# Kernel optimization log

Measured on AMD Instinct MI355X. Metric: run time of the kernel, lower is better.

The kernel has to match this reference:

```python
import jax, jax.numpy as jnp
import numpy as np

NUM_HEADS = 12
SCALE = 0.125  # (C // num_heads) ** -0.5 = 64 ** -0.5


def setup_inputs() -> dict:
    key = jax.random.key(0)
    k1, k2, k3, k4, k5 = jax.random.split(key, 5)
    B, N, C = 8, 1024, 768
    x = jax.random.normal(k1, (B, N, C), dtype=jnp.float32)
    qkv_w = jax.random.normal(k2, (3 * C, C), dtype=jnp.float32) * (C ** -0.5)
    qkv_b = jax.random.normal(k3, (3 * C,), dtype=jnp.float32) * 0.02
    proj_w = jax.random.normal(k4, (C, C), dtype=jnp.float32) * (C ** -0.5)
    proj_b = jax.random.normal(k5, (C,), dtype=jnp.float32) * 0.02
    return {"x": x, "qkv_w": qkv_w, "qkv_b": qkv_b,
            "proj_w": proj_w, "proj_b": proj_b, "H": 32, "W": 32}


def reference(x, qkv_w, qkv_b, proj_w, proj_b, H, W):
    B, N, C = x.shape
    hd = C // NUM_HEADS
    # qkv: [B, N, 3C] -> [3, B, heads, N, hd]
    qkv = (x @ qkv_w.T + qkv_b).reshape(B, N, 3, NUM_HEADS, hd)
    qkv = jnp.transpose(qkv, (2, 0, 3, 1, 4))
    q, k, v = qkv[0], qkv[1], qkv[2]
    # attention scores [B, heads, N, N]
    attn = jnp.einsum('bhnd,bhmd->bhnm', q, k) * SCALE
    attn = jax.nn.softmax(attn, axis=-1)
    # attn_drop / proj_drop are identity in eval mode
    out = jnp.einsum('bhnm,bhmd->bhnd', attn, v)
    out = jnp.transpose(out, (0, 2, 1, 3)).reshape(B, N, C)
    out = out @ proj_w.T + proj_b
    return out
```

## Files before the change

kernel.cpp:

```cpp
#include <hip/hip_runtime.h>
#include <math.h>

#define NSEQ  1024
#define CDIM  768
#define NH    12
#define HD    64
#define QS    6291456
#define EXPC  0.18033688011112042f

typedef __bf16 bf16x8 __attribute__((ext_vector_type(8)));
typedef float  f32x4  __attribute__((ext_vector_type(4)));

__device__ __forceinline__ unsigned short f2bf(float f) {
    union { float f; unsigned u; } v; v.f = f;
    unsigned r = v.u + 0x7FFFu + ((v.u >> 16) & 1u);
    return (unsigned short)(r >> 16);
}

#if __has_builtin(__builtin_amdgcn_cvt_pk_bf16_f32)
typedef __bf16 bf16x2 __attribute__((ext_vector_type(2)));
__device__ __forceinline__ void store_p4(unsigned short* pr, int row16,
                                         float p0, float p1, float p2, float p3) {
    union { bf16x2 v; unsigned u; } a, b;
    a.v = __builtin_amdgcn_cvt_pk_bf16_f32(p0, p1);
    b.v = __builtin_amdgcn_cvt_pk_bf16_f32(p2, p3);
    pr[row16]      = (unsigned short)(a.u);
    pr[16 + row16] = (unsigned short)(a.u >> 16);
    pr[32 + row16] = (unsigned short)(b.u);
    pr[48 + row16] = (unsigned short)(b.u >> 16);
}
#else
__device__ __forceinline__ void store_p4(unsigned short* pr, int row16,
                                         float p0, float p1, float p2, float p3) {
    pr[row16]      = f2bf(p0);
    pr[16 + row16] = f2bf(p1);
    pr[32 + row16] = f2bf(p2);
    pr[48 + row16] = f2bf(p3);
}
#endif

__device__ __forceinline__ void gld_lds16(const unsigned short* g, unsigned short* l) {
    __builtin_amdgcn_global_load_lds(
        (const __attribute__((address_space(1))) void*)g,
        (__attribute__((address_space(3))) void*)l, 16, 0, 0);
}

__global__ __launch_bounds__(256) void cvt_all(const float* __restrict__ x,
                                               const float* __restrict__ w1,
                                               const float* __restrict__ w2,
                                               unsigned short* __restrict__ xb,
                                               unsigned short* __restrict__ w1b,
                                               unsigned short* __restrict__ w2b,
                                               int n0, int n1, int n2) {
    int i = (blockIdx.x * 256 + threadIdx.x) * 4;
    const float* s; unsigned short* d; int off;
    if (i < n0)           { s = x;  d = xb;  off = i; }
    else if (i < n0 + n1) { s = w1; d = w1b; off = i - n0; }
    else if (i < n0 + n1 + n2) { s = w2; d = w2b; off = i - n0 - n1; }
    else return;
    float4 v = *(const float4*)(s + off);
    ushort4 o;
    o.x = f2bf(v.x); o.y = f2bf(v.y); o.z = f2bf(v.z); o.w = f2bf(v.w);
    *(ushort4*)(d + off) = o;
}

template <int MODE>
__global__ __launch_bounds__(256) void mfma_gemm_bt(const unsigned short* __restrict__ A,
                                                    const unsigned short* __restrict__ Bw,
                                                    const float* __restrict__ bias,
                                                    void* __restrict__ outp,
                                                    int M, int N, int K) {
    __shared__ unsigned short smem[4 * 128 * 32];

    const int tid = threadIdx.x;
    const int wave = tid >> 6, lane = tid & 63;
    const int row16 = lane & 15, quad = lane >> 4;
    const int wm = (wave >> 1) * 64, wn = (wave & 1) * 64;
    const int m0 = blockIdx.x * 128, n0 = blockIdx.y * 128;

    const int srow0 = (tid * 8) >> 5,         scol0 = (tid * 8) & 31;
    const int srow1 = ((tid + 256) * 8) >> 5, scol1 = ((tid + 256) * 8) & 31;

    f32x4 acc[4][4];
#pragma unroll
    for (int i = 0; i < 4; ++i)
#pragma unroll
        for (int j = 0; j < 4; ++j) acc[i][j] = (f32x4){0.f, 0.f, 0.f, 0.f};

    gld_lds16(&A[(size_t)(m0 + srow0) * K + scol0], &smem[wave * 512]);
    gld_lds16(&A[(size_t)(m0 + srow1) * K + scol1], &smem[2048 + wave * 512]);
    gld_lds16(&Bw[(size_t)(n0 + srow0) * K + scol0], &smem[8192 + wave * 512]);
    gld_lds16(&Bw[(size_t)(n0 + srow1) * K + scol1], &smem[8192 + 2048 + wave * 512]);

    const int nk = K / 32;
    for (int ki = 0; ki < nk; ++ki) {
        const int co = (ki & 1) * 4096;
        const int no = 4096 - co;
        __syncthreads();
        if (ki + 1 < nk) {
            const int k0 = (ki + 1) * 32;
            gld_lds16(&A[(size_t)(m0 + srow0) * K + k0 + scol0], &smem[no + wave * 512]);
            gld_lds16(&A[(size_t)(m0 + srow1) * K + k0 + scol1], &smem[no + 2048 + wave * 512]);
            gld_lds16(&Bw[(size_t)(n0 + srow0) * K + k0 + scol0], &smem[8192 + no + wave * 512]);
            gld_lds16(&Bw[(size_t)(n0 + srow1) * K + k0 + scol1], &smem[8192 + no + 2048 + wave * 512]);
        }
        bf16x8 af[4], bfr[4];
#pragma unroll
        for (int mt = 0; mt < 4; ++mt)
            af[mt] = *(const bf16x8*)&smem[co + (wm + mt * 16 + row16) * 32 + quad * 8];
#pragma unroll
        for (int nt = 0; nt < 4; ++nt)
            bfr[nt] = *(const bf16x8*)&smem[8192 + co + (wn + nt * 16 + row16) * 32 + quad * 8];
#pragma unroll
        for (int mt = 0; mt < 4; ++mt)
#pragma unroll
            for (int nt = 0; nt < 4; ++nt)
                acc[mt][nt] = __builtin_amdgcn_mfma_f32_16x16x32_bf16(af[mt], bfr[nt], acc[mt][nt], 0, 0, 0);
    }

    float bias4[4];
#pragma unroll
    for (int nt = 0; nt < 4; ++nt) bias4[nt] = bias[n0 + wn + nt * 16 + row16];

    if (MODE == 0) {
#pragma unroll
        for (int mt = 0; mt < 4; ++mt)
#pragma unroll
            for (int nt = 0; nt < 4; ++nt)
#pragma unroll
                for (int r = 0; r < 4; ++r) {
                    int grow = m0 + wm + mt * 16 + quad * 4 + r;
                    int gcol = n0 + wn + nt * 16 + row16;
                    ((float*)outp)[(size_t)grow * N + gcol] = acc[mt][nt][r] + bias4[nt];
                }
    } else {
        unsigned short* qkvb = (unsigned short*)outp;
        __syncthreads();
#pragma unroll
        for (int mt = 0; mt < 4; ++mt)
#pragma unroll
            for (int nt = 0; nt < 4; ++nt)
#pragma unroll
                for (int r = 0; r < 4; ++r)
                    smem[(wm + mt * 16 + quad * 4 + r) * 128 + wn + nt * 16 + row16] =
                        f2bf(acc[mt][nt][r] + bias4[nt]);
        __syncthreads();
#pragma unroll
        for (int i = 0; i < 8; ++i) {
            int u4 = i * 256 + tid;
            int row = u4 >> 4;
            int c8 = u4 & 15;
            int grow = m0 + row;
            int gcol = n0 + c8 * 8;
            int t = gcol / CDIM;
            int rr = gcol - t * CDIM;
            int h = rr >> 6, d = rr & 63;
            int b = grow >> 10, n = grow & 1023;
            *(uint4*)&qkvb[(size_t)t * QS + ((((size_t)b * NH + h) << 10) + n) * 64 + d] =
                *(const uint4*)&smem[row * 128 + c8 * 8];
        }
    }
}

__global__ __launch_bounds__(256, 4) void attn_mfma(const unsigned short* __restrict__ qkv,
                                                    unsigned short* __restrict__ abuf) {
    __shared__ unsigned short Ks[64 * 72];
    __shared__ unsigned short Vt[64 * 72];
    __shared__ unsigned short Ps[4][32 * 72];

    const int tid = threadIdx.x;
    const int wave = tid >> 6, lane = tid & 63;
    const int row16 = lane & 15, quad = lane >> 4;
    const int bid = blockIdx.x;
    const int xcd = bid & 7;
    const int local = bid >> 3;
    const int bh = xcd * 12 + (local >> 3);
    const int qt = local & 7;

    const unsigned short* Qg = qkv + (size_t)bh * NSEQ * HD + (size_t)qt * 128 * HD;
    const unsigned short* Kg = qkv + (size_t)QS + (size_t)bh * NSEQ * HD;
    const unsigned short* Vg = qkv + (size_t)2 * QS + (size_t)bh * NSEQ * HD;

    bf16x8 aq[2][2];
#pragma unroll
    for (int mt = 0; mt < 2; ++mt)
#pragma unroll
        for (int kst = 0; kst < 2; ++kst)
            aq[mt][kst] = *(const bf16x8*)&Qg[(size_t)(wave * 32 + mt * 16 + row16) * 64 +
                                              kst * 32 + quad * 8];

    f32x4 o[2][4];
    float l_i[2][4];
#pragma unroll
    for (int mt = 0; mt < 2; ++mt)
#pragma unroll
        for (int j = 0; j < 4; ++j) {
            o[mt][j] = (f32x4){0.f, 0.f, 0.f, 0.f};
            l_i[mt][j] = 0.f;
        }

    const int krow0 = (tid * 8) >> 6,  kcol0 = (tid * 8) & 63;
    const int krow1 = ((tid + 256) * 8) >> 6, kcol1 = ((tid + 256) * 8) & 63;
    const int kpair = tid & 31;
    const int colc = tid >> 5;

    uint4 ka = *(const uint4*)&Kg[(size_t)krow0 * 64 + kcol0];
    uint4 kb = *(const uint4*)&Kg[(size_t)krow1 * 64 + kcol1];
    uint4 va = *(const uint4*)&Vg[(size_t)(2 * kpair) * 64 + colc * 8];
    uint4 vb = *(const uint4*)&Vg[(size_t)(2 * kpair + 1) * 64 + colc * 8];

    for (int kt = 0; kt < 16; ++kt) {
        __syncthreads();
        *(uint4*)&Ks[krow0 * 72 + kcol0] = ka;
        *(uint4*)&Ks[krow1 * 72 + kcol1] = kb;
        {
            const unsigned short* a16 = (const unsigned short*)&va;
            const unsigned short* b16 = (const unsigned short*)&vb;
            unsigned int* vt32 = (unsigned int*)Vt;
#pragma unroll
            for (int j = 0; j < 8; ++j)
                vt32[(colc * 8 + j) * 36 + kpair] =
                    (unsigned int)a16[j] | ((unsigned int)b16[j] << 16);
        }
        __syncthreads();

        if (kt < 15) {
            const unsigned short* kn = Kg + (size_t)(kt + 1) * 64 * 64;
            const unsigned short* vn = Vg + (size_t)(kt + 1) * 64 * 64;
            ka = *(const uint4*)&kn[(size_t)krow0 * 64 + kcol0];
            kb = *(const uint4*)&kn[(size_t)krow1 * 64 + kcol1];
            va = *(const uint4*)&vn[(size_t)(2 * kpair) * 64 + colc * 8];
            vb = *(const uint4*)&vn[(size_t)(2 * kpair + 1) * 64 + colc * 8];
        }

        f32x4 s[2][4];
#pragma unroll
        for (int mt = 0; mt < 2; ++mt)
#pragma unroll
            for (int nt = 0; nt < 4; ++nt) s[mt][nt] = (f32x4){0.f, 0.f, 0.f, 0.f};
#pragma unroll
        for (int kst = 0; kst < 2; ++kst) {
            bf16x8 bk[4];
#pragma unroll
            for (int nt = 0; nt < 4; ++nt)
                bk[nt] = *(const bf16x8*)&Ks[(nt * 16 + row16) * 72 + kst * 32 + quad * 8];
#pragma unroll
            for (int mt = 0; mt < 2; ++mt)
#pragma unroll
                for (int nt = 0; nt < 4; ++nt)
                    s[mt][nt] = __builtin_amdgcn_mfma_f32_16x16x32_bf16(aq[mt][kst], bk[nt], s[mt][nt], 0, 0, 0);
        }

#pragma unroll
        for (int mt = 0; mt < 2; ++mt)
#pragma unroll
            for (int r = 0; r < 4; ++r) {
                float p0 = __builtin_amdgcn_exp2f(s[mt][0][r] * EXPC);
                float p1 = __builtin_amdgcn_exp2f(s[mt][1][r] * EXPC);
                float p2 = __builtin_amdgcn_exp2f(s[mt][2][r] * EXPC);
                float p3 = __builtin_amdgcn_exp2f(s[mt][3][r] * EXPC);
                l_i[mt][r] += (p0 + p1) + (p2 + p3);
                store_p4(&Ps[wave][(mt * 16 + quad * 4 + r) * 72], row16, p0, p1, p2, p3);
            }

#pragma unroll
        for (int kst = 0; kst < 2; ++kst) {
            bf16x8 ap[2], bv[4];
#pragma unroll
            for (int mt = 0; mt < 2; ++mt)
                ap[mt] = *(const bf16x8*)&Ps[wave][(mt * 16 + row16) * 72 + kst * 32 + quad * 8];
#pragma unroll
            for (int dt = 0; dt < 4; ++dt)
                bv[dt] = *(const bf16x8*)&Vt[(dt * 16 + row16) * 72 + kst * 32 + quad * 8];
#pragma unroll
            for (int mt = 0; mt < 2; ++mt)
#pragma unroll
                for (int dt = 0; dt < 4; ++dt)
                    o[mt][dt] = __builtin_amdgcn_mfma_f32_16x16x32_bf16(ap[mt], bv[dt], o[mt][dt], 0, 0, 0);
        }
    }

    const int b = bh / NH, h = bh - b * NH;
#pragma unroll
    for (int mt = 0; mt < 2; ++mt)
#pragma unroll
        for (int r = 0; r < 4; ++r) {
            float l = l_i[mt][r];
            l += __shfl_xor(l, 1);
            l += __shfl_xor(l, 2);
            l += __shfl_xor(l, 4);
            l += __shfl_xor(l, 8);
            float inv = 1.f / l;
            int n = qt * 128 + wave * 32 + mt * 16 + quad * 4 + r;
            size_t base = ((size_t)(b * NSEQ + n)) * CDIM + h * HD;
#pragma unroll
            for (int dt = 0; dt < 4; ++dt)
                abuf[base + dt * 16 + row16] = f2bf(o[mt][dt][r] * inv);
        }
}

extern "C" void kernel_launch(void* const* d_in, const int* in_sizes, int n_in,
                              void* d_out, int out_size, void* d_ws, size_t ws_size,
                              hipStream_t stream) {
    const float* x      = (const float*)d_in[0];
    const float* qkv_w  = (const float*)d_in[1];
    const float* qkv_b  = (const float*)d_in[2];
    const float* proj_w = (const float*)d_in[3];
    const float* proj_b = (const float*)d_in[4];
    float* out = (float*)d_out;

    const int M = 8 * NSEQ;
    unsigned short* ws = (unsigned short*)d_ws;
    unsigned short* xb   = ws;
    unsigned short* wq   = xb + (size_t)M * CDIM;
    unsigned short* wp   = wq + (size_t)3 * CDIM * CDIM;
    unsigned short* qkvb = wp + (size_t)CDIM * CDIM;
    unsigned short* ab   = qkvb + (size_t)3 * QS;

    const int nx = M * CDIM, nq = 3 * CDIM * CDIM, np = CDIM * CDIM;
    cvt_all<<<(nx + nq + np) / 1024, 256, 0, stream>>>(x, qkv_w, proj_w, xb, wq, wp,
                                                       nx, nq, np);

    mfma_gemm_bt<1><<<dim3(M / 128, (3 * CDIM) / 128), 256, 0, stream>>>(
        xb, wq, qkv_b, qkvb, M, 3 * CDIM, CDIM);

    attn_mfma<<<dim3(8 * NH * (NSEQ / 128)), 256, 0, stream>>>(qkvb, ab);

    mfma_gemm_bt<0><<<dim3(M / 128, CDIM / 128), 256, 0, stream>>>(
        ab, wp, proj_b, out, M, CDIM, CDIM);
}
```

Before: 195.6 us.

## Use 256x128 tiles for QKV GEMM and transpose attention score MFMA for packed P stores

Splits the GEMM template into a projection kernel and a dedicated QKV kernel. The QKV kernel uses 256x128 block tiles with each wave computing 64x128, which gives more B-tile reuse but uses more accumulator registers. The epilogue writes to LDS in two passes. In attention, S is computed as K·Q^T so each lane holds four consecutive key columns, allowing packed 8-byte stores of P to LDS instead of scattered 2-byte stores. The row-sum reduction changes to match the new layout.

```diff
diff --git a/kernel.cpp b/kernel.cpp
--- a/kernel.cpp
+++ b/kernel.cpp
@@ -19,23 +19,16 @@
 
 #if __has_builtin(__builtin_amdgcn_cvt_pk_bf16_f32)
 typedef __bf16 bf16x2 __attribute__((ext_vector_type(2)));
-__device__ __forceinline__ void store_p4(unsigned short* pr, int row16,
-                                         float p0, float p1, float p2, float p3) {
+__device__ __forceinline__ uint2 pack4bf(float p0, float p1, float p2, float p3) {
     union { bf16x2 v; unsigned u; } a, b;
     a.v = __builtin_amdgcn_cvt_pk_bf16_f32(p0, p1);
     b.v = __builtin_amdgcn_cvt_pk_bf16_f32(p2, p3);
-    pr[row16]      = (unsigned short)(a.u);
-    pr[16 + row16] = (unsigned short)(a.u >> 16);
-    pr[32 + row16] = (unsigned short)(b.u);
-    pr[48 + row16] = (unsigned short)(b.u >> 16);
+    return make_uint2(a.u, b.u);
 }
 #else
-__device__ __forceinline__ void store_p4(unsigned short* pr, int row16,
-                                         float p0, float p1, float p2, float p3) {
-    pr[row16]      = f2bf(p0);
-    pr[16 + row16] = f2bf(p1);
-    pr[32 + row16] = f2bf(p2);
-    pr[48 + row16] = f2bf(p3);
+__device__ __forceinline__ uint2 pack4bf(float p0, float p1, float p2, float p3) {
+    return make_uint2((unsigned)f2bf(p0) | ((unsigned)f2bf(p1) << 16),
+                      (unsigned)f2bf(p2) | ((unsigned)f2bf(p3) << 16));
 }
 #endif
 
@@ -64,12 +57,11 @@
     *(ushort4*)(d + off) = o;
 }
 
-template <int MODE>
-__global__ __launch_bounds__(256) void mfma_gemm_bt(const unsigned short* __restrict__ A,
-                                                    const unsigned short* __restrict__ Bw,
-                                                    const float* __restrict__ bias,
-                                                    void* __restrict__ outp,
-                                                    int M, int N, int K) {
+__global__ __launch_bounds__(256) void gemm_proj(const unsigned short* __restrict__ A,
+                                                 const unsigned short* __restrict__ Bw,
+                                                 const float* __restrict__ bias,
+                                                 float* __restrict__ out,
+                                                 int M, int N, int K) {
     __shared__ unsigned short smem[4 * 128 * 32];
 
     const int tid = threadIdx.x;
@@ -122,35 +114,107 @@
 #pragma unroll
     for (int nt = 0; nt < 4; ++nt) bias4[nt] = bias[n0 + wn + nt * 16 + row16];
 
-    if (MODE == 0) {
+#pragma unroll
+    for (int mt = 0; mt < 4; ++mt)
+#pragma unroll
+        for (int nt = 0; nt < 4; ++nt)
+#pragma unroll
+            for (int r = 0; r < 4; ++r) {
+                int grow = m0 + wm + mt * 16 + quad * 4 + r;
+                int gcol = n0 + wn + nt * 16 + row16;
+                out[(size_t)grow * N + gcol] = acc[mt][nt][r] + bias4[nt];
+            }
+}
+
+__global__ __launch_bounds__(256) void gemm_qkv(const unsigned short* __restrict__ A,
+                                                const unsigned short* __restrict__ Bw,
+                                                const float* __restrict__ bias,
+                                                unsigned short* __restrict__ qkvb,
+                                                int M, int N, int K) {
+    __shared__ unsigned short smem[2 * 12288];
+
+    const int tid = threadIdx.x;
+    const int wave = tid >> 6, lane = tid & 63;
+    const int row16 = lane & 15, quad = lane >> 4;
+    const int m0 = blockIdx.x * 256, n0 = blockIdx.y * 128;
+
+    f32x4 acc[4][8];
+#pragma unroll
+    for (int i = 0; i < 4; ++i)
+#pragma unroll
+        for (int j = 0; j < 8; ++j) acc[i][j] = (f32x4){0.f, 0.f, 0.f, 0.f};
+
+#pragma unroll
+    for (int i = 0; i < 4; ++i) {
+        const int flat = (tid + i * 256) * 8;
+        gld_lds16(&A[(size_t)(m0 + (flat >> 5)) * K + (flat & 31)],
+                  &smem[i * 2048 + wave * 512]);
+    }
+#pragma unroll
+    for (int i = 0; i < 2; ++i) {
+        const int flat = (tid + i * 256) * 8;
+        gld_lds16(&Bw[(size_t)(n0 + (flat >> 5)) * K + (flat & 31)],
+                  &smem[8192 + i * 2048 + wave * 512]);
+    }
+
+    const int nk = K / 32;
+    for (int ki = 0; ki < nk; ++ki) {
+        const int co = (ki & 1) * 12288;
+        const int no = 12288 - co;
+        __syncthreads();
+        if (ki + 1 < nk) {
+            const int k0 = (ki + 1) * 32;
+#pragma unroll
+            for (int i = 0; i < 4; ++i) {
+                const int flat = (tid + i * 256) * 8;
+                gld_lds16(&A[(size_t)(m0 + (flat >> 5)) * K + k0 + (flat & 31)],
+                          &smem[no + i * 2048 + wave * 512]);
+            }
+#pragma unroll
+            for (int i = 0; i < 2; ++i) {
+                const int flat = (tid + i * 256) * 8;
+                gld_lds16(&Bw[(size_t)(n0 + (flat >> 5)) * K + k0 + (flat & 31)],
+                          &smem[no + 8192 + i * 2048 + wave * 512]);
+            }
+        }
+        bf16x8 af[4], bfr[8];
 #pragma unroll
         for (int mt = 0; mt < 4; ++mt)
-#pragma unroll
-            for (int nt = 0; nt < 4; ++nt)
-#pragma unroll
-                for (int r = 0; r < 4; ++r) {
-                    int grow = m0 + wm + mt * 16 + quad * 4 + r;
-                    int gcol = n0 + wn + nt * 16 + row16;
-                    ((float*)outp)[(size_t)grow * N + gcol] = acc[mt][nt][r] + bias4[nt];
-                }
-    } else {
-        unsigned short* qkvb = (unsigned short*)outp;
-        __syncthreads();
+            af[mt] = *(const bf16x8*)&smem[co + (wave * 64 + mt * 16 + row16) * 32 + quad * 8];
+#pragma unroll
+        for (int nt = 0; nt < 8; ++nt)
+            bfr[nt] = *(const bf16x8*)&smem[co + 8192 + (nt * 16 + row16) * 32 + quad * 8];
 #pragma unroll
         for (int mt = 0; mt < 4; ++mt)
 #pragma unroll
-            for (int nt = 0; nt < 4; ++nt)
-#pragma unroll
-                for (int r = 0; r < 4; ++r)
-                    smem[(wm + mt * 16 + quad * 4 + r) * 128 + wn + nt * 16 + row16] =
-                        f2bf(acc[mt][nt][r] + bias4[nt]);
+            for (int nt = 0; nt < 8; ++nt)
+                acc[mt][nt] = __builtin_amdgcn_mfma_f32_16x16x32_bf16(af[mt], bfr[nt], acc[mt][nt], 0, 0, 0);
+    }
+
+    float bias8[8];
+#pragma unroll
+    for (int nt = 0; nt < 8; ++nt) bias8[nt] = bias[n0 + nt * 16 + row16];
+
+#pragma unroll
+    for (int p = 0; p < 2; ++p) {
+        __syncthreads();
+        if ((wave >> 1) == p) {
+#pragma unroll
+            for (int mt = 0; mt < 4; ++mt)
+#pragma unroll
+                for (int nt = 0; nt < 8; ++nt)
+#pragma unroll
+                    for (int r = 0; r < 4; ++r)
+                        smem[((wave & 1) * 64 + mt * 16 + quad * 4 + r) * 128 + nt * 16 + row16] =
+                            f2bf(acc[mt][nt][r] + bias8[nt]);
+        }
         __syncthreads();
 #pragma unroll
         for (int i = 0; i < 8; ++i) {
             int u4 = i * 256 + tid;
             int row = u4 >> 4;
             int c8 = u4 & 15;
-            int grow = m0 + row;
+            int grow = m0 + p * 128 + row;
             int gcol = n0 + c8 * 8;
             int t = gcol / CDIM;
             int rr = gcol - t * CDIM;
@@ -190,14 +254,11 @@
                                               kst * 32 + quad * 8];
 
     f32x4 o[2][4];
-    float l_i[2][4];
+    float l_i[2] = {0.f, 0.f};
 #pragma unroll
     for (int mt = 0; mt < 2; ++mt)
 #pragma unroll
-        for (int j = 0; j < 4; ++j) {
-            o[mt][j] = (f32x4){0.f, 0.f, 0.f, 0.f};
-            l_i[mt][j] = 0.f;
-        }
+        for (int j = 0; j < 4; ++j) o[mt][j] = (f32x4){0.f, 0.f, 0.f, 0.f};
 
     const int krow0 = (tid * 8) >> 6,  kcol0 = (tid * 8) & 63;
     const int krow1 = ((tid + 256) * 8) >> 6, kcol1 = ((tid + 256) * 8) & 63;
@@ -233,34 +294,35 @@
             vb = *(const uint4*)&vn[(size_t)(2 * kpair + 1) * 64 + colc * 8];
         }
 
-        f32x4 s[2][4];
+        f32x4 st[4][2];
+#pragma unroll
+        for (int nt = 0; nt < 4; ++nt)
+#pragma unroll
+            for (int mt = 0; mt < 2; ++mt) st[nt][mt] = (f32x4){0.f, 0.f, 0.f, 0.f};
+#pragma unroll
+        for (int kst = 0; kst < 2; ++kst) {
+            bf16x8 ak[4];
+#pragma unroll
+            for (int nt = 0; nt < 4; ++nt)
+                ak[nt] = *(const bf16x8*)&Ks[(nt * 16 + row16) * 72 + kst * 32 + quad * 8];
+#pragma unroll
+            for (int nt = 0; nt < 4; ++nt)
+#pragma unroll
+                for (int mt = 0; mt < 2; ++mt)
+                    st[nt][mt] = __builtin_amdgcn_mfma_f32_16x16x32_bf16(ak[nt], aq[mt][kst], st[nt][mt], 0, 0, 0);
+        }
+
 #pragma unroll
         for (int mt = 0; mt < 2; ++mt)
 #pragma unroll
-            for (int nt = 0; nt < 4; ++nt) s[mt][nt] = (f32x4){0.f, 0.f, 0.f, 0.f};
-#pragma unroll
-        for (int kst = 0; kst < 2; ++kst) {
-            bf16x8 bk[4];
-#pragma unroll
-            for (int nt = 0; nt < 4; ++nt)
-                bk[nt] = *(const bf16x8*)&Ks[(nt * 16 + row16) * 72 + kst * 32 + quad * 8];
-#pragma unroll
-            for (int mt = 0; mt < 2; ++mt)
-#pragma unroll
-                for (int nt = 0; nt < 4; ++nt)
-                    s[mt][nt] = __builtin_amdgcn_mfma_f32_16x16x32_bf16(aq[mt][kst], bk[nt], s[mt][nt], 0, 0, 0);
-        }
-
-#pragma unroll
-        for (int mt = 0; mt < 2; ++mt)
-#pragma unroll
-            for (int r = 0; r < 4; ++r) {
-                float p0 = __builtin_amdgcn_exp2f(s[mt][0][r] * EXPC);
-                float p1 = __builtin_amdgcn_exp2f(s[mt][1][r] * EXPC);
-                float p2 = __builtin_amdgcn_exp2f(s[mt][2][r] * EXPC);
-                float p3 = __builtin_amdgcn_exp2f(s[mt][3][r] * EXPC);
-                l_i[mt][r] += (p0 + p1) + (p2 + p3);
-                store_p4(&Ps[wave][(mt * 16 + quad * 4 + r) * 72], row16, p0, p1, p2, p3);
+            for (int nt = 0; nt < 4; ++nt) {
+                float p0 = __builtin_amdgcn_exp2f(st[nt][mt][0] * EXPC);
+                float p1 = __builtin_amdgcn_exp2f(st[nt][mt][1] * EXPC);
+                float p2 = __builtin_amdgcn_exp2f(st[nt][mt][2] * EXPC);
+                float p3 = __builtin_amdgcn_exp2f(st[nt][mt][3] * EXPC);
+                l_i[mt] += (p0 + p1) + (p2 + p3);
+                *(uint2*)&Ps[wave][(mt * 16 + row16) * 72 + nt * 16 + quad * 4] =
+                    pack4bf(p0, p1, p2, p3);
             }
 
 #pragma unroll
@@ -282,21 +344,20 @@
 
     const int b = bh / NH, h = bh - b * NH;
 #pragma unroll
-    for (int mt = 0; mt < 2; ++mt)
+    for (int mt = 0; mt < 2; ++mt) {
+        float l = l_i[mt];
+        l += __shfl_xor(l, 16);
+        l += __shfl_xor(l, 32);
 #pragma unroll
         for (int r = 0; r < 4; ++r) {
-            float l = l_i[mt][r];
-            l += __shfl_xor(l, 1);
-            l += __shfl_xor(l, 2);
-            l += __shfl_xor(l, 4);
-            l += __shfl_xor(l, 8);
-            float inv = 1.f / l;
+            float inv = 1.f / __shfl(l, quad * 4 + r);
             int n = qt * 128 + wave * 32 + mt * 16 + quad * 4 + r;
             size_t base = ((size_t)(b * NSEQ + n)) * CDIM + h * HD;
 #pragma unroll
             for (int dt = 0; dt < 4; ++dt)
                 abuf[base + dt * 16 + row16] = f2bf(o[mt][dt][r] * inv);
         }
+    }
 }
 
 extern "C" void kernel_launch(void* const* d_in, const int* in_sizes, int n_in,
@@ -321,11 +382,11 @@
     cvt_all<<<(nx + nq + np) / 1024, 256, 0, stream>>>(x, qkv_w, proj_w, xb, wq, wp,
                                                        nx, nq, np);
 
-    mfma_gemm_bt<1><<<dim3(M / 128, (3 * CDIM) / 128), 256, 0, stream>>>(
+    gemm_qkv<<<dim3(M / 256, (3 * CDIM) / 128), 256, 0, stream>>>(
         xb, wq, qkv_b, qkvb, M, 3 * CDIM, CDIM);
 
     attn_mfma<<<dim3(8 * NH * (NSEQ / 128)), 256, 0, stream>>>(qkvb, ab);
 
-    mfma_gemm_bt<0><<<dim3(M / 128, CDIM / 128), 256, 0, stream>>>(
+    gemm_proj<<<dim3(M / 128, CDIM / 128), 256, 0, stream>>>(
         ab, wp, proj_b, out, M, CDIM, CDIM);
 }
```

Result: slower. 217.1 us (+11.0%).
